# Kernel tuning notes

Measured on AMD Instinct MI355X. Metric: run time of the kernel, lower is better.

Reference implementation:

```python
import jax, jax.numpy as jnp
import numpy as np

IN_F = 256
OUT_F = 256
ALPHA = 0.2  # leakyrelu negative slope


def setup_inputs() -> dict:
    key = jax.random.key(0)
    k1, k2, k3 = jax.random.split(key, 3)
    B, N = 64, 1024
    x_loc = jax.random.normal(k1, (B, N, IN_F), dtype=jnp.float32)
    # xavier_uniform with gain=1.414
    def xavier(k, shape, gain=1.414):
        fan_in, fan_out = shape[0], shape[1]
        bound = gain * np.sqrt(6.0 / (fan_in + fan_out))
        return jax.random.uniform(k, shape, jnp.float32, -bound, bound)
    W = xavier(k2, (IN_F, OUT_F))
    a = xavier(k3, (2 * OUT_F, 1))
    return {"x_loc": x_loc, "W": W, "a": a, "entity_num": N}


def reference(x_loc, W, a, entity_num):
    # h: [B, N, F]
    h = jnp.matmul(x_loc, W)
    F_out = W.shape[1]
    a1 = a[:F_out, 0]   # [F]
    a2 = a[F_out:, 0]   # [F]
    # score(i, j) = leakyrelu(a1 . h_i + a2 . h_j)  -- decomposition of
    # matmul(cat(h_i, h_j), a); identical math, avoids O(N^2 * 2F) tensor.
    s1 = jnp.einsum('bnf,f->bn', h, a1)  # [B, N]
    s2 = jnp.einsum('bnf,f->bn', h, a2)  # [B, N]
    e = s1[:, :, None] + s2[:, None, :]  # [B, N, N]
    e = jnp.where(e > 0, e, ALPHA * e)   # leakyrelu(alpha=0.2)
    attention = jax.nn.softmax(e, axis=2)
    h_prime = jnp.matmul(attention, h)   # [B, N, F]
    return h_prime  # concat=False -> no elu
```

## Files before the change

kernel.cpp:

```cpp
#include <hip/hip_runtime.h>


typedef unsigned short u16;
typedef unsigned int   u32;
typedef float  f32x4  __attribute__((ext_vector_type(4)));
typedef __bf16 bf16x8 __attribute__((ext_vector_type(8)));
typedef __bf16 bf16x4 __attribute__((ext_vector_type(4)));

#define NB    64
#define NENT  1024
#define FD    256
#define NROWS (NB * NENT)
#define ALPHA 0.2f
#define LOG2E 1.4426950408889634f

typedef __attribute__((address_space(1))) const void* gas_ptr;
typedef __attribute__((address_space(3))) void*       las_ptr;
__device__ __forceinline__ void gload16(const void* g, void* l) {
  __builtin_amdgcn_global_load_lds((gas_ptr)g, (las_ptr)l, 16, 0, 0);
}
__device__ __forceinline__ float fexp2(float x) {
  float r;
  asm("v_exp_f32 %0, %1" : "=v"(r) : "v"(x));
  return r;
}

__global__ __launch_bounds__(256) void k_wa(const float* __restrict__ W,
                                            const float* __restrict__ a,
                                            float* __restrict__ Wa1,
                                            float* __restrict__ Wa2) {
  const int k = blockIdx.x, f = threadIdx.x;
  const float w = W[(size_t)k * FD + f];
  float p1 = w * a[f];
  float p2 = w * a[FD + f];
#pragma unroll
  for (int off = 1; off < 64; off <<= 1) {
    p1 += __shfl_xor(p1, off, 64);
    p2 += __shfl_xor(p2, off, 64);
  }
  __shared__ float r1[4], r2[4];
  const int wv = f >> 6, lane = f & 63;
  if (lane == 0) { r1[wv] = p1; r2[wv] = p2; }
  __syncthreads();
  if (f == 0) {
    Wa1[k] = r1[0] + r1[1] + r1[2] + r1[3];
    Wa2[k] = r2[0] + r2[1] + r2[2] + r2[3];
  }
}

__global__ __launch_bounds__(256) void k_wt(const float* __restrict__ W,
                                            u16* __restrict__ Wt) {
  __shared__ float tile[64][65];
  const int t = threadIdx.x;
  const int ki = blockIdx.x >> 2, fi = blockIdx.x & 3;
  const int k0 = ki * 64, f0 = fi * 64;
  const int r = t >> 4, c4 = (t & 15) * 4;
#pragma unroll
  for (int it = 0; it < 4; ++it) {
    const int row = r + it * 16;
    float4 v = *(const float4*)&W[(size_t)(k0 + row) * FD + f0 + c4];
    tile[row][c4 + 0] = v.x; tile[row][c4 + 1] = v.y;
    tile[row][c4 + 2] = v.z; tile[row][c4 + 3] = v.w;
  }
  __syncthreads();
#pragma unroll
  for (int it = 0; it < 4; ++it) {
    const int fr = r + it * 16;
    bf16x4 pk;
    pk[0] = (__bf16)tile[c4 + 0][fr]; pk[1] = (__bf16)tile[c4 + 1][fr];
    pk[2] = (__bf16)tile[c4 + 2][fr]; pk[3] = (__bf16)tile[c4 + 3][fr];
    *(bf16x4*)&Wt[(size_t)(f0 + fr) * FD + k0 + c4] = pk;
  }
}

__global__ __launch_bounds__(512, 2) void k_h(
    const float* __restrict__ x, const u16* __restrict__ Wt,
    const float* __restrict__ Wa1g, const float* __restrict__ Wa2g,
    u16* __restrict__ h_oct, float* __restrict__ s1, float* __restrict__ s2) {
  __shared__ __align__(16) u16 A_lds[2][4][256][8];
  __shared__ __align__(16) u16 B_lds[2][4][256][8];
  __shared__ float wa1[FD], wa2[FD];
  const int t = threadIdx.x;
  const int lane = t & 63, wv = t >> 6;
  const int wr = wv >> 2, wc = wv & 3;
  const int g16 = lane >> 4, c15 = lane & 15;
  const int p = blockIdx.x;
  const int lb = (p & 7) * 32 + (p >> 3);
  const int rT = lb * 256;
  if (t < FD) { wa1[t] = Wa1g[t]; wa2[t] = Wa2g[t]; }
  const int row = t >> 1, half = t & 1;
  const float* xsrc = x + (size_t)(rT + row) * FD + half * 16;
  float p1 = 0.f, p2 = 0.f;
  f32x4 acc[8][4];
  const f32x4 vz = {0.f, 0.f, 0.f, 0.f};
#pragma unroll
  for (int i = 0; i < 8; ++i)
#pragma unroll
    for (int j = 0; j < 4; ++j) acc[i][j] = vz;

  auto stage = [&](int nb, int kc, const float4& f0, const float4& f1,
                   const float4& f2, const float4& f3) {
    const int k0n = kc * 32;
    const int d0 = t;
    gload16(Wt + (size_t)(d0 & 255) * FD + k0n + (d0 >> 8) * 8,
            (char*)(&B_lds[nb][0][0][0]) + d0 * 16);
    const int d1 = t + 512;
    gload16(Wt + (size_t)(d1 & 255) * FD + k0n + (d1 >> 8) * 8,
            (char*)(&B_lds[nb][0][0][0]) + d1 * 16);
    bf16x8 w0, w1;
    w0[0] = (__bf16)f0.x; w0[1] = (__bf16)f0.y;
    w0[2] = (__bf16)f0.z; w0[3] = (__bf16)f0.w;
    w0[4] = (__bf16)f1.x; w0[5] = (__bf16)f1.y;
    w0[6] = (__bf16)f1.z; w0[7] = (__bf16)f1.w;
    w1[0] = (__bf16)f2.x; w1[1] = (__bf16)f2.y;
    w1[2] = (__bf16)f2.z; w1[3] = (__bf16)f2.w;
    w1[4] = (__bf16)f3.x; w1[5] = (__bf16)f3.y;
    w1[6] = (__bf16)f3.z; w1[7] = (__bf16)f3.w;
    *(bf16x8*)&A_lds[nb][half * 2][row][0] = w0;
    *(bf16x8*)&A_lds[nb][half * 2 + 1][row][0] = w1;
    const int kb = k0n + half * 16;
    p1 += f0.x*wa1[kb+ 0] + f0.y*wa1[kb+ 1] + f0.z*wa1[kb+ 2] + f0.w*wa1[kb+ 3]
        + f1.x*wa1[kb+ 4] + f1.y*wa1[kb+ 5] + f1.z*wa1[kb+ 6] + f1.w*wa1[kb+ 7]
        + f2.x*wa1[kb+ 8] + f2.y*wa1[kb+ 9] + f2.z*wa1[kb+10] + f2.w*wa1[kb+11]
        + f3.x*wa1[kb+12] + f3.y*wa1[kb+13] + f3.z*wa1[kb+14] + f3.w*wa1[kb+15];
    p2 += f0.x*wa2[kb+ 0] + f0.y*wa2[kb+ 1] + f0.z*wa2[kb+ 2] + f0.w*wa2[kb+ 3]
        + f1.x*wa2[kb+ 4] + f1.y*wa2[kb+ 5] + f1.z*wa2[kb+ 6] + f1.w*wa2[kb+ 7]
        + f2.x*wa2[kb+ 8] + f2.y*wa2[kb+ 9] + f2.z*wa2[kb+10] + f2.w*wa2[kb+11]
        + f3.x*wa2[kb+12] + f3.y*wa2[kb+13] + f3.z*wa2[kb+14] + f3.w*wa2[kb+15];
  };
  auto mfma_step = [&](int cb) {
    bf16x8 bfv[4];
#pragma unroll
    for (int fj = 0; fj < 4; ++fj)
      bfv[fj] = *(const bf16x8*)&B_lds[cb][g16][wc * 64 + fj * 16 + c15][0];
#pragma unroll
    for (int fi = 0; fi < 8; ++fi) {
      bf16x8 af = *(const bf16x8*)&A_lds[cb][g16][wr * 128 + fi * 16 + c15][0];
#pragma unroll
      for (int fj = 0; fj < 4; ++fj)
        acc[fi][fj] = __builtin_amdgcn_mfma_f32_16x16x32_bf16(
            af, bfv[fj], acc[fi][fj], 0, 0, 0);
    }
  };

  float4 xc0 = *(const float4*)(xsrc +  0);
  float4 xc1 = *(const float4*)(xsrc +  4);
  float4 xc2 = *(const float4*)(xsrc +  8);
  float4 xc3 = *(const float4*)(xsrc + 12);
  float4 xb0 = *(const float4*)(xsrc + 32);
  float4 xb1 = *(const float4*)(xsrc + 36);
  float4 xb2 = *(const float4*)(xsrc + 40);
  float4 xb3 = *(const float4*)(xsrc + 44);
  float4 xa0 = *(const float4*)(xsrc + 64);
  float4 xa1 = *(const float4*)(xsrc + 68);
  float4 xa2 = *(const float4*)(xsrc + 72);
  float4 xa3 = *(const float4*)(xsrc + 76);
  __syncthreads();
  stage(0, 0, xc0, xc1, xc2, xc3);
  __syncthreads();
#pragma unroll 1
  for (int ks2 = 0; ks2 < 4; ++ks2) {
    stage(1, 2 * ks2 + 1, xb0, xb1, xb2, xb3);
    if (2 * ks2 + 3 < 8) {
      const float* s = xsrc + (2 * ks2 + 3) * 32;
      xb0 = *(const float4*)(s);      xb1 = *(const float4*)(s + 4);
      xb2 = *(const float4*)(s + 8);  xb3 = *(const float4*)(s + 12);
    }
    mfma_step(0);
    __syncthreads();
    if (2 * ks2 + 2 < 8) {
      stage(0, 2 * ks2 + 2, xa0, xa1, xa2, xa3);
      if (2 * ks2 + 4 < 8) {
        const float* s = xsrc + (2 * ks2 + 4) * 32;
        xa0 = *(const float4*)(s);      xa1 = *(const float4*)(s + 4);
        xa2 = *(const float4*)(s + 8);  xa3 = *(const float4*)(s + 12);
      }
    }
    mfma_step(1);
    __syncthreads();
  }
  p1 += __shfl_xor(p1, 1, 64);
  p2 += __shfl_xor(p2, 1, 64);
  if (half == 0) { s1[rT + row] = p1; s2[rT + row] = p2; }
#pragma unroll
  for (int fi = 0; fi < 8; ++fi) {
    const int rowb = rT + wr * 128 + fi * 16 + 4 * g16;
    const int oct = rowb >> 3, u = rowb & 7;
#pragma unroll
    for (int fj = 0; fj < 4; ++fj) {
      const int col = wc * 64 + fj * 16 + c15;
      bf16x4 pk;
      pk[0] = (__bf16)acc[fi][fj][0]; pk[1] = (__bf16)acc[fi][fj][1];
      pk[2] = (__bf16)acc[fi][fj][2]; pk[3] = (__bf16)acc[fi][fj][3];
      *(bf16x4*)((u16*)h_oct + ((size_t)oct * FD + col) * 8 + u) = pk;
    }
  }
}

__global__ __launch_bounds__(512, 2) void k_pv(
    const u16* __restrict__ h_oct, const float* __restrict__ s1,
    const float* __restrict__ s2, float* __restrict__ out) {
  __shared__ __align__(16) u16 P_lds[2][4][256][8];
  __shared__ __align__(16) u16 V_lds[2][4][256][8];
  __shared__ float s2l[NENT];
  const int t = threadIdx.x;
  const int lane = t & 63, wv = t >> 6;
  const int wr = wv >> 2, wc = wv & 3;
  const int g16 = lane >> 4, c15 = lane & 15;
  const int p = blockIdx.x;
  const int lb = (p & 7) * 32 + (p >> 3);
  const int b = lb >> 2, itile = lb & 3;
  const int i0 = itile * 256;
  const int irow = t & 255, gsl = t >> 8;
  const int rowg = b * NENT + i0 + irow;
  const float s1v = s1[rowg];
  const size_t obase = (size_t)b * (NENT / 8);
  f32x4 acc[8][4];
  const f32x4 vz = {0.f, 0.f, 0.f, 0.f};
#pragma unroll
  for (int i = 0; i < 8; ++i)
#pragma unroll
    for (int j = 0; j < 4; ++j) acc[i][j] = vz;
  float zsum = 0.f;

  auto vload = [&](int nb, int ksn) {
    const int j0n = ksn * 32;
    const int d0 = t;
    gload16(h_oct + ((obase + (j0n >> 3) + (d0 >> 8)) * FD + (d0 & 255)) * 8,
            (char*)(&V_lds[nb][0][0][0]) + d0 * 16);
    const int d1 = t + 512;
    gload16(h_oct + ((obase + (j0n >> 3) + (d1 >> 8)) * FD + (d1 & 255)) * 8,
            (char*)(&V_lds[nb][0][0][0]) + d1 * 16);
  };

  vload(0, 0);
  *(float2*)&s2l[t * 2] = *(const float2*)&s2[(size_t)b * NENT + t * 2];
  __syncthreads();
  float sm = s2l[lane];
#pragma unroll
  for (int j = 1; j < 16; ++j) sm = fmaxf(sm, s2l[lane + j * 64]);
#pragma unroll
  for (int off = 1; off < 64; off <<= 1) sm = fmaxf(sm, __shfl_xor(sm, off, 64));
  const float q = s1v + sm;
  const float mv = fmaxf(q, ALPHA * q);
  const float C2v = ALPHA * LOG2E;
  const float mvC = mv * LOG2E;
  const float s1A = s1v * LOG2E - mvC;
  const float s1B = s1v * C2v - mvC;

  auto genp = [&](int nb, int ksn) {
    const int jb = ksn * 32 + gsl * 16;
    float4 qa = *(const float4*)&s2l[jb];
    float4 qb = *(const float4*)&s2l[jb + 4];
    float4 qc = *(const float4*)&s2l[jb + 8];
    float4 qd = *(const float4*)&s2l[jb + 12];
    float zp = 0.f;
    auto pg = [&](float s2j) -> float {
      float vA = fmaf(s2j, LOG2E, s1A);
      float vB = fmaf(s2j, C2v, s1B);
      float r = fexp2(fmaxf(vA, vB));
      zp += r;
      return r;
    };
    bf16x8 pw0, pw1;
    pw0[0] = (__bf16)pg(qa.x); pw0[1] = (__bf16)pg(qa.y);
    pw0[2] = (__bf16)pg(qa.z); pw0[3] = (__bf16)pg(qa.w);
    pw0[4] = (__bf16)pg(qb.x); pw0[5] = (__bf16)pg(qb.y);
    pw0[6] = (__bf16)pg(qb.z); pw0[7] = (__bf16)pg(qb.w);
    pw1[0] = (__bf16)pg(qc.x); pw1[1] = (__bf16)pg(qc.y);
    pw1[2] = (__bf16)pg(qc.z); pw1[3] = (__bf16)pg(qc.w);
    pw1[4] = (__bf16)pg(qd.x); pw1[5] = (__bf16)pg(qd.y);
    pw1[6] = (__bf16)pg(qd.z); pw1[7] = (__bf16)pg(qd.w);
    zsum += zp;
    *(bf16x8*)&P_lds[nb][2 * gsl][irow][0] = pw0;
    *(bf16x8*)&P_lds[nb][2 * gsl + 1][irow][0] = pw1;
  };
  auto mfma_step = [&](int cb) {
    bf16x8 bfv[4];
#pragma unroll
    for (int fj = 0; fj < 4; ++fj)
      bfv[fj] = *(const bf16x8*)&V_lds[cb][g16][wc * 64 + fj * 16 + c15][0];
#pragma unroll
    for (int fi = 0; fi < 8; ++fi) {
      bf16x8 af = *(const bf16x8*)&P_lds[cb][g16][wr * 128 + fi * 16 + c15][0];
#pragma unroll
      for (int fj = 0; fj < 4; ++fj)
        acc[fi][fj] = __builtin_amdgcn_mfma_f32_16x16x32_bf16(
            af, bfv[fj], acc[fi][fj], 0, 0, 0);
    }
  };

  genp(0, 0);
  __syncthreads();
#pragma unroll 1
  for (int ks2 = 0; ks2 < 16; ++ks2) {
    vload(1, 2 * ks2 + 1);
    genp(1, 2 * ks2 + 1);
    mfma_step(0);
    __syncthreads();
    if (2 * ks2 + 2 < 32) {
      vload(0, 2 * ks2 + 2);
      genp(0, 2 * ks2 + 2);
    }
    mfma_step(1);
    __syncthreads();
  }
  float* zred = (float*)&P_lds[0][0][0][0];
  zred[gsl * 256 + irow] = zsum;
  __syncthreads();
#pragma unroll
  for (int fi = 0; fi < 8; ++fi) {
    const int rloc = wr * 128 + fi * 16 + 4 * g16;
    float rz[4];
#pragma unroll
    for (int r = 0; r < 4; ++r)
      rz[r] = __builtin_amdgcn_rcpf(zred[rloc + r] + zred[256 + rloc + r]);
#pragma unroll
    for (int fj = 0; fj < 4; ++fj) {
      const int col = wc * 64 + fj * 16 + c15;
      float* o = out + ((size_t)b * NENT + i0 + rloc) * FD + col;
      o[0 * FD] = acc[fi][fj][0] * rz[0];
      o[1 * FD] = acc[fi][fj][1] * rz[1];
      o[2 * FD] = acc[fi][fj][2] * rz[2];
      o[3 * FD] = acc[fi][fj][3] * rz[3];
    }
  }
}

extern "C" void kernel_launch(void* const* d_in, const int* in_sizes, int n_in,
                              void* d_out, int out_size, void* d_ws, size_t ws_size,
                              hipStream_t stream) {
  const float* x = (const float*)d_in[0];
  const float* W = (const float*)d_in[1];
  const float* a = (const float*)d_in[2];
  float* out = (float*)d_out;

  char* ws = (char*)d_ws;
  u16*   h_oct = (u16*)ws;
  float* s1  = (float*)(ws + (size_t)33554432);
  float* s2  = s1 + NROWS;
  float* Wa1 = s2 + NROWS;
  float* Wa2 = Wa1 + FD;
  u16*   Wt  = (u16*)(Wa2 + FD);

  k_wa<<<dim3(256), dim3(256), 0, stream>>>(W, a, Wa1, Wa2);
  k_wt<<<dim3(16), dim3(256), 0, stream>>>(W, Wt);
  k_h<<<dim3(256), dim3(512), 0, stream>>>(x, Wt, Wa1, Wa2, h_oct, s1, s2);
  k_pv<<<dim3(256), dim3(512), 0, stream>>>(h_oct, s1, s2, out);
}
```

Before: 78.62 us.

## Deepen software pipelining with explicit waitcnt barriers and triple-buffered V tiles

Result: slower. 83.09 us (+5.7%).

```diff
diff --git a/kernel.cpp b/kernel.cpp
--- a/kernel.cpp
+++ b/kernel.cpp
@@ -13,6 +13,15 @@
 #define NROWS (NB * NENT)
 #define ALPHA 0.2f
 #define LOG2E 1.4426950408889634f
+
+#define VMCNT(n)  asm volatile("s_waitcnt vmcnt(" #n ")" ::: "memory")
+#define LGKMCNT0  asm volatile("s_waitcnt lgkmcnt(0)" ::: "memory")
+#define BAR()                                                                  \
+  do {                                                                         \
+    __builtin_amdgcn_s_barrier();                                              \
+    asm volatile("" ::: "memory");                                             \
+    __builtin_amdgcn_sched_barrier(0);                                         \
+  } while (0)
 
 typedef __attribute__((address_space(1))) const void* gas_ptr;
 typedef __attribute__((address_space(3))) void*       las_ptr;
@@ -87,7 +96,6 @@
   const int p = blockIdx.x;
   const int lb = (p & 7) * 32 + (p >> 3);
   const int rT = lb * 256;
-  if (t < FD) { wa1[t] = Wa1g[t]; wa2[t] = Wa2g[t]; }
   const int row = t >> 1, half = t & 1;
   const float* xsrc = x + (size_t)(rT + row) * FD + half * 16;
   float p1 = 0.f, p2 = 0.f;
@@ -98,8 +106,7 @@
 #pragma unroll
     for (int j = 0; j < 4; ++j) acc[i][j] = vz;
 
-  auto stage = [&](int nb, int kc, const float4& f0, const float4& f1,
-                   const float4& f2, const float4& f3) {
+  auto issueB = [&](int nb, int kc) {
     const int k0n = kc * 32;
     const int d0 = t;
     gload16(Wt + (size_t)(d0 & 255) * FD + k0n + (d0 >> 8) * 8,
@@ -107,32 +114,39 @@
     const int d1 = t + 512;
     gload16(Wt + (size_t)(d1 & 255) * FD + k0n + (d1 >> 8) * 8,
             (char*)(&B_lds[nb][0][0][0]) + d1 * 16);
+  };
+  auto stageA = [&](int nb, int kc, const float4* xr) {
     bf16x8 w0, w1;
-    w0[0] = (__bf16)f0.x; w0[1] = (__bf16)f0.y;
-    w0[2] = (__bf16)f0.z; w0[3] = (__bf16)f0.w;
-    w0[4] = (__bf16)f1.x; w0[5] = (__bf16)f1.y;
-    w0[6] = (__bf16)f1.z; w0[7] = (__bf16)f1.w;
-    w1[0] = (__bf16)f2.x; w1[1] = (__bf16)f2.y;
-    w1[2] = (__bf16)f2.z; w1[3] = (__bf16)f2.w;
-    w1[4] = (__bf16)f3.x; w1[5] = (__bf16)f3.y;
-    w1[6] = (__bf16)f3.z; w1[7] = (__bf16)f3.w;
+    w0[0] = (__bf16)xr[0].x; w0[1] = (__bf16)xr[0].y;
+    w0[2] = (__bf16)xr[0].z; w0[3] = (__bf16)xr[0].w;
+    w0[4] = (__bf16)xr[1].x; w0[5] = (__bf16)xr[1].y;
+    w0[6] = (__bf16)xr[1].z; w0[7] = (__bf16)xr[1].w;
+    w1[0] = (__bf16)xr[2].x; w1[1] = (__bf16)xr[2].y;
+    w1[2] = (__bf16)xr[2].z; w1[3] = (__bf16)xr[2].w;
+    w1[4] = (__bf16)xr[3].x; w1[5] = (__bf16)xr[3].y;
+    w1[6] = (__bf16)xr[3].z; w1[7] = (__bf16)xr[3].w;
     *(bf16x8*)&A_lds[nb][half * 2][row][0] = w0;
     *(bf16x8*)&A_lds[nb][half * 2 + 1][row][0] = w1;
-    const int kb = k0n + half * 16;
-    p1 += f0.x*wa1[kb+ 0] + f0.y*wa1[kb+ 1] + f0.z*wa1[kb+ 2] + f0.w*wa1[kb+ 3]
-        + f1.x*wa1[kb+ 4] + f1.y*wa1[kb+ 5] + f1.z*wa1[kb+ 6] + f1.w*wa1[kb+ 7]
-        + f2.x*wa1[kb+ 8] + f2.y*wa1[kb+ 9] + f2.z*wa1[kb+10] + f2.w*wa1[kb+11]
-        + f3.x*wa1[kb+12] + f3.y*wa1[kb+13] + f3.z*wa1[kb+14] + f3.w*wa1[kb+15];
-    p2 += f0.x*wa2[kb+ 0] + f0.y*wa2[kb+ 1] + f0.z*wa2[kb+ 2] + f0.w*wa2[kb+ 3]
-        + f1.x*wa2[kb+ 4] + f1.y*wa2[kb+ 5] + f1.z*wa2[kb+ 6] + f1.w*wa2[kb+ 7]
-        + f2.x*wa2[kb+ 8] + f2.y*wa2[kb+ 9] + f2.z*wa2[kb+10] + f2.w*wa2[kb+11]
-        + f3.x*wa2[kb+12] + f3.y*wa2[kb+13] + f3.z*wa2[kb+14] + f3.w*wa2[kb+15];
+    const int kb = kc * 32 + half * 16;
+#pragma unroll
+    for (int q = 0; q < 4; ++q) {
+      p1 += xr[q].x * wa1[kb + 4 * q + 0] + xr[q].y * wa1[kb + 4 * q + 1] +
+            xr[q].z * wa1[kb + 4 * q + 2] + xr[q].w * wa1[kb + 4 * q + 3];
+      p2 += xr[q].x * wa2[kb + 4 * q + 0] + xr[q].y * wa2[kb + 4 * q + 1] +
+            xr[q].z * wa2[kb + 4 * q + 2] + xr[q].w * wa2[kb + 4 * q + 3];
+    }
+  };
+  auto loadx = [&](float4* xr, int kc) {
+    const float* s = xsrc + kc * 32;
+    xr[0] = *(const float4*)(s);      xr[1] = *(const float4*)(s + 4);
+    xr[2] = *(const float4*)(s + 8);  xr[3] = *(const float4*)(s + 12);
   };
   auto mfma_step = [&](int cb) {
     bf16x8 bfv[4];
 #pragma unroll
     for (int fj = 0; fj < 4; ++fj)
       bfv[fj] = *(const bf16x8*)&B_lds[cb][g16][wc * 64 + fj * 16 + c15][0];
+    __builtin_amdgcn_s_setprio(1);
 #pragma unroll
     for (int fi = 0; fi < 8; ++fi) {
       bf16x8 af = *(const bf16x8*)&A_lds[cb][g16][wr * 128 + fi * 16 + c15][0];
@@ -141,43 +155,36 @@
         acc[fi][fj] = __builtin_amdgcn_mfma_f32_16x16x32_bf16(
             af, bfv[fj], acc[fi][fj], 0, 0, 0);
     }
-  };
-
-  float4 xc0 = *(const float4*)(xsrc +  0);
-  float4 xc1 = *(const float4*)(xsrc +  4);
-  float4 xc2 = *(const float4*)(xsrc +  8);
-  float4 xc3 = *(const float4*)(xsrc + 12);
-  float4 xb0 = *(const float4*)(xsrc + 32);
-  float4 xb1 = *(const float4*)(xsrc + 36);
-  float4 xb2 = *(const float4*)(xsrc + 40);
-  float4 xb3 = *(const float4*)(xsrc + 44);
-  float4 xa0 = *(const float4*)(xsrc + 64);
-  float4 xa1 = *(const float4*)(xsrc + 68);
-  float4 xa2 = *(const float4*)(xsrc + 72);
-  float4 xa3 = *(const float4*)(xsrc + 76);
-  __syncthreads();
-  stage(0, 0, xc0, xc1, xc2, xc3);
-  __syncthreads();
-#pragma unroll 1
-  for (int ks2 = 0; ks2 < 4; ++ks2) {
-    stage(1, 2 * ks2 + 1, xb0, xb1, xb2, xb3);
-    if (2 * ks2 + 3 < 8) {
-      const float* s = xsrc + (2 * ks2 + 3) * 32;
-      xb0 = *(const float4*)(s);      xb1 = *(const float4*)(s + 4);
-      xb2 = *(const float4*)(s + 8);  xb3 = *(const float4*)(s + 12);
-    }
-    mfma_step(0);
-    __syncthreads();
-    if (2 * ks2 + 2 < 8) {
-      stage(0, 2 * ks2 + 2, xa0, xa1, xa2, xa3);
-      if (2 * ks2 + 4 < 8) {
-        const float* s = xsrc + (2 * ks2 + 4) * 32;
-        xa0 = *(const float4*)(s);      xa1 = *(const float4*)(s + 4);
-        xa2 = *(const float4*)(s + 8);  xa3 = *(const float4*)(s + 12);
-      }
-    }
-    mfma_step(1);
-    __syncthreads();
+    __builtin_amdgcn_s_setprio(0);
+  };
+
+  if (t < FD) { wa1[t] = Wa1g[t]; wa2[t] = Wa2g[t]; }
+  float4 xe[4], xo[4];
+  loadx(xe, 0);
+  loadx(xo, 1);
+  issueB(0, 0);
+  LGKMCNT0;
+  BAR();
+  stageA(0, 0, xe);
+  loadx(xe, 2);
+  LGKMCNT0;
+  VMCNT(4);
+  BAR();
+
+#pragma unroll
+  for (int k = 0; k < 8; ++k) {
+    if (k < 7) {
+      issueB((k + 1) & 1, k + 1);
+      float4* xr = (k & 1) ? xe : xo;
+      stageA((k + 1) & 1, k + 1, xr);
+      if (k + 3 < 8) loadx(xr, k + 3);
+    }
+    mfma_step(k & 1);
+    if (k < 7) {
+      LGKMCNT0;
+      if (k + 3 < 8) VMCNT(4); else VMCNT(0);
+      BAR();
+    }
   }
   p1 += __shfl_xor(p1, 1, 64);
   p2 += __shfl_xor(p2, 1, 64);
@@ -201,7 +208,7 @@
     const u16* __restrict__ h_oct, const float* __restrict__ s1,
     const float* __restrict__ s2, float* __restrict__ out) {
   __shared__ __align__(16) u16 P_lds[2][4][256][8];
-  __shared__ __align__(16) u16 V_lds[2][4][256][8];
+  __shared__ __align__(16) u16 V_lds[3][4][256][8];
   __shared__ float s2l[NENT];
   const int t = threadIdx.x;
   const int lane = t & 63, wv = t >> 6;
@@ -213,7 +220,6 @@
   const int i0 = itile * 256;
   const int irow = t & 255, gsl = t >> 8;
   const int rowg = b * NENT + i0 + irow;
-  const float s1v = s1[rowg];
   const size_t obase = (size_t)b * (NENT / 8);
   f32x4 acc[8][4];
   const f32x4 vz = {0.f, 0.f, 0.f, 0.f};
@@ -233,9 +239,13 @@
             (char*)(&V_lds[nb][0][0][0]) + d1 * 16);
   };
 
+  const float s1v = s1[rowg];
+  float2 s2f = *(const float2*)&s2[(size_t)b * NENT + t * 2];
   vload(0, 0);
-  *(float2*)&s2l[t * 2] = *(const float2*)&s2[(size_t)b * NENT + t * 2];
-  __syncthreads();
+  vload(1, 1);
+  *(float2*)&s2l[t * 2] = s2f;
+  LGKMCNT0;
+  BAR();
   float sm = s2l[lane];
 #pragma unroll
   for (int j = 1; j < 16; ++j) sm = fmaxf(sm, s2l[lane + j * 64]);
@@ -275,36 +285,44 @@
     *(bf16x8*)&P_lds[nb][2 * gsl][irow][0] = pw0;
     *(bf16x8*)&P_lds[nb][2 * gsl + 1][irow][0] = pw1;
   };
-  auto mfma_step = [&](int cb) {
+  auto mfma_step = [&](int pb, int vb) {
     bf16x8 bfv[4];
 #pragma unroll
     for (int fj = 0; fj < 4; ++fj)
-      bfv[fj] = *(const bf16x8*)&V_lds[cb][g16][wc * 64 + fj * 16 + c15][0];
+      bfv[fj] = *(const bf16x8*)&V_lds[vb][g16][wc * 64 + fj * 16 + c15][0];
+    __builtin_amdgcn_s_setprio(1);
 #pragma unroll
     for (int fi = 0; fi < 8; ++fi) {
-      bf16x8 af = *(const bf16x8*)&P_lds[cb][g16][wr * 128 + fi * 16 + c15][0];
+      bf16x8 af = *(const bf16x8*)&P_lds[pb][g16][wr * 128 + fi * 16 + c15][0];
 #pragma unroll
       for (int fj = 0; fj < 4; ++fj)
         acc[fi][fj] = __builtin_amdgcn_mfma_f32_16x16x32_bf16(
             af, bfv[fj], acc[fi][fj], 0, 0, 0);
     }
+    __builtin_amdgcn_s_setprio(0);
   };
 
   genp(0, 0);
+  LGKMCNT0;
+  VMCNT(2);
+  BAR();
+
+  int rb = 0, wb = 2;
+#pragma unroll 1
+  for (int k = 0; k < 32; ++k) {
+    if (k < 30) vload(wb, k + 2);
+    if (k < 31) genp((k + 1) & 1, k + 1);
+    mfma_step(k & 1, rb);
+    if (k < 31) {
+      LGKMCNT0;
+      if (k < 30) VMCNT(2);
+      else        VMCNT(0);
+      BAR();
+    }
+    rb = (rb == 2) ? 0 : rb + 1;
+    wb = (wb == 2) ? 0 : wb + 1;
+  }
   __syncthreads();
-#pragma unroll 1
-  for (int ks2 = 0; ks2 < 16; ++ks2) {
-    vload(1, 2 * ks2 + 1);
-    genp(1, 2 * ks2 + 1);
-    mfma_step(0);
-    __syncthreads();
-    if (2 * ks2 + 2 < 32) {
-      vload(0, 2 * ks2 + 2);
-      genp(0, 2 * ks2 + 2);
-    }
-    mfma_step(1);
-    __syncthreads();
-  }
   float* zred = (float*)&P_lds[0][0][0][0];
   zred[gsl * 256 + irow] = zsum;
   __syncthreads();
```

## Replace quadratic attention with sorted prefix-sum scan over rank-one scores

Applied to the files above, without the earlier changes.

Result: slower. 192.1 us (+144.3%).

```diff
diff --git a/kernel.cpp b/kernel.cpp
--- a/kernel.cpp
+++ b/kernel.cpp
@@ -12,17 +12,11 @@
 #define FD    256
 #define NROWS (NB * NENT)
 #define ALPHA 0.2f
-#define LOG2E 1.4426950408889634f
 
 typedef __attribute__((address_space(1))) const void* gas_ptr;
 typedef __attribute__((address_space(3))) void*       las_ptr;
 __device__ __forceinline__ void gload16(const void* g, void* l) {
   __builtin_amdgcn_global_load_lds((gas_ptr)g, (las_ptr)l, 16, 0, 0);
-}
-__device__ __forceinline__ float fexp2(float x) {
-  float r;
-  asm("v_exp_f32 %0, %1" : "=v"(r) : "v"(x));
-  return r;
 }
 
 __global__ __launch_bounds__(256) void k_wa(const float* __restrict__ W,
@@ -76,10 +70,12 @@
 __global__ __launch_bounds__(512, 2) void k_h(
     const float* __restrict__ x, const u16* __restrict__ Wt,
     const float* __restrict__ Wa1g, const float* __restrict__ Wa2g,
-    u16* __restrict__ h_oct, float* __restrict__ s1, float* __restrict__ s2) {
-  __shared__ __align__(16) u16 A_lds[2][4][256][8];
-  __shared__ __align__(16) u16 B_lds[2][4][256][8];
-  __shared__ float wa1[FD], wa2[FD];
+    u16* __restrict__ h, float* __restrict__ s1, float* __restrict__ s2) {
+  __shared__ __align__(16) char smem[67584];
+  u16* Ab = (u16*)smem;
+  u16* Bb = (u16*)(smem + 32768);
+  float* wa1 = (float*)(smem + 65536);
+  float* wa2 = wa1 + FD;
   const int t = threadIdx.x;
   const int lane = t & 63, wv = t >> 6;
   const int wr = wv >> 2, wc = wv & 3;
@@ -103,10 +99,10 @@
     const int k0n = kc * 32;
     const int d0 = t;
     gload16(Wt + (size_t)(d0 & 255) * FD + k0n + (d0 >> 8) * 8,
-            (char*)(&B_lds[nb][0][0][0]) + d0 * 16);
+            (char*)Bb + nb * 8192 * 2 + d0 * 16);
     const int d1 = t + 512;
     gload16(Wt + (size_t)(d1 & 255) * FD + k0n + (d1 >> 8) * 8,
-            (char*)(&B_lds[nb][0][0][0]) + d1 * 16);
+            (char*)Bb + nb * 8192 * 2 + d1 * 16);
     bf16x8 w0, w1;
     w0[0] = (__bf16)f0.x; w0[1] = (__bf16)f0.y;
     w0[2] = (__bf16)f0.z; w0[3] = (__bf16)f0.w;
@@ -116,8 +112,8 @@
     w1[2] = (__bf16)f2.z; w1[3] = (__bf16)f2.w;
     w1[4] = (__bf16)f3.x; w1[5] = (__bf16)f3.y;
     w1[6] = (__bf16)f3.z; w1[7] = (__bf16)f3.w;
-    *(bf16x8*)&A_lds[nb][half * 2][row][0] = w0;
-    *(bf16x8*)&A_lds[nb][half * 2 + 1][row][0] = w1;
+    *(bf16x8*)(Ab + ((nb * 4 + half * 2) * 256 + row) * 8) = w0;
+    *(bf16x8*)(Ab + ((nb * 4 + half * 2 + 1) * 256 + row) * 8) = w1;
     const int kb = k0n + half * 16;
     p1 += f0.x*wa1[kb+ 0] + f0.y*wa1[kb+ 1] + f0.z*wa1[kb+ 2] + f0.w*wa1[kb+ 3]
         + f1.x*wa1[kb+ 4] + f1.y*wa1[kb+ 5] + f1.z*wa1[kb+ 6] + f1.w*wa1[kb+ 7]
@@ -132,10 +128,10 @@
     bf16x8 bfv[4];
 #pragma unroll
     for (int fj = 0; fj < 4; ++fj)
-      bfv[fj] = *(const bf16x8*)&B_lds[cb][g16][wc * 64 + fj * 16 + c15][0];
+      bfv[fj] = *(const bf16x8*)(Bb + ((cb * 4 + g16) * 256 + wc * 64 + fj * 16 + c15) * 8);
 #pragma unroll
     for (int fi = 0; fi < 8; ++fi) {
-      bf16x8 af = *(const bf16x8*)&A_lds[cb][g16][wr * 128 + fi * 16 + c15][0];
+      bf16x8 af = *(const bf16x8*)(Ab + ((cb * 4 + g16) * 256 + wr * 128 + fi * 16 + c15) * 8);
 #pragma unroll
       for (int fj = 0; fj < 4; ++fj)
         acc[fi][fj] = __builtin_amdgcn_mfma_f32_16x16x32_bf16(
@@ -182,147 +178,224 @@
   p1 += __shfl_xor(p1, 1, 64);
   p2 += __shfl_xor(p2, 1, 64);
   if (half == 0) { s1[rT + row] = p1; s2[rT + row] = p2; }
-#pragma unroll
-  for (int fi = 0; fi < 8; ++fi) {
-    const int rowb = rT + wr * 128 + fi * 16 + 4 * g16;
-    const int oct = rowb >> 3, u = rowb & 7;
-#pragma unroll
-    for (int fj = 0; fj < 4; ++fj) {
-      const int col = wc * 64 + fj * 16 + c15;
-      bf16x4 pk;
-      pk[0] = (__bf16)acc[fi][fj][0]; pk[1] = (__bf16)acc[fi][fj][1];
-      pk[2] = (__bf16)acc[fi][fj][2]; pk[3] = (__bf16)acc[fi][fj][3];
-      *(bf16x4*)((u16*)h_oct + ((size_t)oct * FD + col) * 8 + u) = pk;
-    }
-  }
-}
-
-__global__ __launch_bounds__(512, 2) void k_pv(
-    const u16* __restrict__ h_oct, const float* __restrict__ s1,
+  u16* ep = (u16*)smem;
+#pragma unroll 1
+  for (int hh = 0; hh < 4; ++hh) {
+    if (wr == (hh >> 1)) {
+#pragma unroll
+      for (int fi2 = 0; fi2 < 4; ++fi2) {
+        const int fi = (hh & 1) * 4 + fi2;
+        const int erow = fi2 * 16 + 4 * g16;
+#pragma unroll
+        for (int fj = 0; fj < 4; ++fj) {
+          const int col = wc * 64 + fj * 16 + c15;
+#pragma unroll
+          for (int r = 0; r < 4; ++r) {
+            __bf16 bv = (__bf16)acc[fi][fj][r];
+            ep[(erow + r) * 264 + col] = __builtin_bit_cast(u16, bv);
+          }
+        }
+      }
+    }
+    __syncthreads();
+    const int rrow = t >> 3, seg = t & 7;
+    const u16* src = ep + rrow * 264 + seg * 32;
+    u16* dst = h + (size_t)(rT + hh * 64 + rrow) * FD + seg * 32;
+#pragma unroll
+    for (int q = 0; q < 4; ++q)
+      *(uint4*)(dst + q * 8) = *(const uint4*)(src + q * 8);
+    __syncthreads();
+  }
+}
+
+__global__ __launch_bounds__(512) void k_sc(
+    const u16* __restrict__ h, const float* __restrict__ s1,
     const float* __restrict__ s2, float* __restrict__ out) {
-  __shared__ __align__(16) u16 P_lds[2][4][256][8];
-  __shared__ __align__(16) u16 V_lds[2][4][256][8];
-  __shared__ float s2l[NENT];
+  __shared__ float key[1024];
+  __shared__ u16   pid[1024];
+  __shared__ float e2l[1024], e2al[1024];
+  __shared__ float Su[1025], Sv[1025];
+  __shared__ float c1l[1024], c2l[1024];
+  __shared__ u32   cnt[1025];
+  __shared__ u16   ibl[1025];
+  __shared__ u16   iol[1024];
+  __shared__ float UpS[8];
+  __shared__ float Up[8][64], Vp[8][64];
   const int t = threadIdx.x;
-  const int lane = t & 63, wv = t >> 6;
-  const int wr = wv >> 2, wc = wv & 3;
-  const int g16 = lane >> 4, c15 = lane & 15;
-  const int p = blockIdx.x;
-  const int lb = (p & 7) * 32 + (p >> 3);
-  const int b = lb >> 2, itile = lb & 3;
-  const int i0 = itile * 256;
-  const int irow = t & 255, gsl = t >> 8;
-  const int rowg = b * NENT + i0 + irow;
-  const float s1v = s1[rowg];
-  const size_t obase = (size_t)b * (NENT / 8);
-  f32x4 acc[8][4];
-  const f32x4 vz = {0.f, 0.f, 0.f, 0.f};
-#pragma unroll
-  for (int i = 0; i < 8; ++i)
-#pragma unroll
-    for (int j = 0; j < 4; ++j) acc[i][j] = vz;
-  float zsum = 0.f;
-
-  auto vload = [&](int nb, int ksn) {
-    const int j0n = ksn * 32;
-    const int d0 = t;
-    gload16(h_oct + ((obase + (j0n >> 3) + (d0 >> 8)) * FD + (d0 & 255)) * 8,
-            (char*)(&V_lds[nb][0][0][0]) + d0 * 16);
-    const int d1 = t + 512;
-    gload16(h_oct + ((obase + (j0n >> 3) + (d1 >> 8)) * FD + (d1 & 255)) * 8,
-            (char*)(&V_lds[nb][0][0][0]) + d1 * 16);
+  const int b = blockIdx.y, fc = blockIdx.x;
+  const int w = t >> 6, lane = t & 63;
+
+  key[t]       = s2[(size_t)b * NENT + t];       pid[t]       = (u16)t;
+  key[t + 512] = s2[(size_t)b * NENT + t + 512]; pid[t + 512] = (u16)(t + 512);
+  __syncthreads();
+  for (int kk = 2; kk <= 1024; kk <<= 1) {
+    for (int j = kk >> 1; j > 0; j >>= 1) {
+      if (j >= 64) __syncthreads();
+      else asm volatile("" ::: "memory");
+      const int i  = ((t & ~(j - 1)) << 1) | (t & (j - 1));
+      const int ix = i | j;
+      const bool up = ((i & kk) == 0);
+      float a = key[i], c = key[ix];
+      u16 pa = pid[i], pc = pid[ix];
+      const bool sw = up ? (a > c) : (a < c);
+      if (sw) { key[i] = c; key[ix] = a; pid[i] = pc; pid[ix] = pa; }
+    }
+  }
+  __syncthreads();
+  {
+    float k0 = key[t], k1 = key[t + 512];
+    e2l[t] = __expf(k0);        e2l[t + 512] = __expf(k1);
+    e2al[t] = __expf(ALPHA * k0); e2al[t + 512] = __expf(ALPHA * k1);
+  }
+  __syncthreads();
+  auto scanx = [&](const float* src, float* dst) {
+    float a = src[2 * t], bb = src[2 * t + 1];
+    float s = a + bb;
+    float inc = s;
+#pragma unroll
+    for (int d = 1; d < 64; d <<= 1) {
+      float o = __shfl_up(inc, d, 64);
+      if (lane >= d) inc += o;
+    }
+    if (lane == 63) UpS[w] = inc;
+    __syncthreads();
+    float woff = 0.f;
+#pragma unroll
+    for (int w2 = 0; w2 < 8; ++w2) { float pv = UpS[w2]; if (w2 < w) woff += pv; }
+    float P = woff + inc - s;
+    dst[2 * t] = P; dst[2 * t + 1] = P + a;
+    if (t == 511) dst[1024] = P + s;
+    __syncthreads();
   };
-
-  vload(0, 0);
-  *(float2*)&s2l[t * 2] = *(const float2*)&s2[(size_t)b * NENT + t * 2];
-  __syncthreads();
-  float sm = s2l[lane];
-#pragma unroll
-  for (int j = 1; j < 16; ++j) sm = fmaxf(sm, s2l[lane + j * 64]);
-#pragma unroll
-  for (int off = 1; off < 64; off <<= 1) sm = fmaxf(sm, __shfl_xor(sm, off, 64));
-  const float q = s1v + sm;
-  const float mv = fmaxf(q, ALPHA * q);
-  const float C2v = ALPHA * LOG2E;
-  const float mvC = mv * LOG2E;
-  const float s1A = s1v * LOG2E - mvC;
-  const float s1B = s1v * C2v - mvC;
-
-  auto genp = [&](int nb, int ksn) {
-    const int jb = ksn * 32 + gsl * 16;
-    float4 qa = *(const float4*)&s2l[jb];
-    float4 qb = *(const float4*)&s2l[jb + 4];
-    float4 qc = *(const float4*)&s2l[jb + 8];
-    float4 qd = *(const float4*)&s2l[jb + 12];
-    float zp = 0.f;
-    auto pg = [&](float s2j) -> float {
-      float vA = fmaf(s2j, LOG2E, s1A);
-      float vB = fmaf(s2j, C2v, s1B);
-      float r = fexp2(fmaxf(vA, vB));
-      zp += r;
-      return r;
-    };
-    bf16x8 pw0, pw1;
-    pw0[0] = (__bf16)pg(qa.x); pw0[1] = (__bf16)pg(qa.y);
-    pw0[2] = (__bf16)pg(qa.z); pw0[3] = (__bf16)pg(qa.w);
-    pw0[4] = (__bf16)pg(qb.x); pw0[5] = (__bf16)pg(qb.y);
-    pw0[6] = (__bf16)pg(qb.z); pw0[7] = (__bf16)pg(qb.w);
-    pw1[0] = (__bf16)pg(qc.x); pw1[1] = (__bf16)pg(qc.y);
-    pw1[2] = (__bf16)pg(qc.z); pw1[3] = (__bf16)pg(qc.w);
-    pw1[4] = (__bf16)pg(qd.x); pw1[5] = (__bf16)pg(qd.y);
-    pw1[6] = (__bf16)pg(qd.z); pw1[7] = (__bf16)pg(qd.w);
-    zsum += zp;
-    *(bf16x8*)&P_lds[nb][2 * gsl][irow][0] = pw0;
-    *(bf16x8*)&P_lds[nb][2 * gsl + 1][irow][0] = pw1;
+  scanx(e2l, Su);
+  scanx(e2al, Sv);
+  const float s2max = key[1023];
+  const float SuN = Su[1024], SvN = Sv[1024];
+  int kfA, kfB;
+  {
+    cnt[t] = 0; cnt[t + 512] = 0;
+    if (t == 0) cnt[1024] = 0;
+  }
+  __syncthreads();
+#pragma unroll
+  for (int hi = 0; hi < 2; ++hi) {
+    const int i = t + hi * 512;
+    const float s1v = s1[(size_t)b * NENT + i];
+    const float th = -s1v;
+    int kf = 0;
+#pragma unroll
+    for (int d = 1024; d >= 1; d >>= 1)
+      if (kf + d <= 1024 && key[kf + d - 1] < th) kf += d;
+    const float qm = s1v + s2max;
+    const float m = fmaxf(qm, ALPHA * qm);
+    const float en1 = __expf(fminf(s1v - m, 80.f));
+    const float en2 = __expf(fminf(ALPHA * s1v - m, 80.f));
+    const float Z = en1 * (SuN - Su[kf]) + en2 * Sv[kf];
+    const float rZ = 1.f / Z;
+    c1l[i] = en1 * rZ; c2l[i] = en2 * rZ;
+    if (hi == 0) kfA = kf; else kfB = kf;
+    atomicAdd(&cnt[kf], 1u);
+  }
+  __syncthreads();
+  {
+    float a = (float)cnt[2 * t], bb = (float)cnt[2 * t + 1];
+    cnt[2 * t] = 0; cnt[2 * t + 1] = 0;
+    if (t == 0) cnt[1024] = 0;
+    float s = a + bb;
+    float inc = s;
+#pragma unroll
+    for (int d = 1; d < 64; d <<= 1) {
+      float o = __shfl_up(inc, d, 64);
+      if (lane >= d) inc += o;
+    }
+    if (lane == 63) UpS[w] = inc;
+    __syncthreads();
+    float woff = 0.f;
+#pragma unroll
+    for (int w2 = 0; w2 < 8; ++w2) { float pv = UpS[w2]; if (w2 < w) woff += pv; }
+    float P = woff + inc - s;
+    ibl[2 * t] = (u16)P; ibl[2 * t + 1] = (u16)(P + a);
+    if (t == 511) ibl[1024] = (u16)(P + s);
+  }
+  __syncthreads();
+  {
+    int pos = (int)ibl[kfA] + (int)atomicAdd(&cnt[kfA], 1u);
+    pos = pos < 1023 ? pos : 1023;
+    iol[pos] = (u16)t;
+    int posB = (int)ibl[kfB] + (int)atomicAdd(&cnt[kfB], 1u);
+    posB = posB < 1023 ? posB : 1023;
+    iol[posB] = (u16)(t + 512);
+  }
+  __syncthreads();
+  const int col = fc * 64 + lane;
+  const u16* hb = h + (size_t)b * NENT * FD + col;
+  const int r0 = w * 128;
+  float ha[8], hc[8];
+  auto ldg8 = [&](float* dstv, int rbase) {
+#pragma unroll
+    for (int u = 0; u < 8; ++u) {
+      u16 raw = hb[(size_t)((int)pid[rbase + u]) * FD];
+      dstv[u] = (float)__builtin_bit_cast(__bf16, raw);
+    }
   };
-  auto mfma_step = [&](int cb) {
-    bf16x8 bfv[4];
-#pragma unroll
-    for (int fj = 0; fj < 4; ++fj)
-      bfv[fj] = *(const bf16x8*)&V_lds[cb][g16][wc * 64 + fj * 16 + c15][0];
-#pragma unroll
-    for (int fi = 0; fi < 8; ++fi) {
-      bf16x8 af = *(const bf16x8*)&P_lds[cb][g16][wr * 128 + fi * 16 + c15][0];
-#pragma unroll
-      for (int fj = 0; fj < 4; ++fj)
-        acc[fi][fj] = __builtin_amdgcn_mfma_f32_16x16x32_bf16(
-            af, bfv[fj], acc[fi][fj], 0, 0, 0);
-    }
-  };
-
-  genp(0, 0);
-  __syncthreads();
+  float U = 0.f, V = 0.f;
+  ldg8(ha, r0);
 #pragma unroll 1
-  for (int ks2 = 0; ks2 < 16; ++ks2) {
-    vload(1, 2 * ks2 + 1);
-    genp(1, 2 * ks2 + 1);
-    mfma_step(0);
-    __syncthreads();
-    if (2 * ks2 + 2 < 32) {
-      vload(0, 2 * ks2 + 2);
-      genp(0, 2 * ks2 + 2);
-    }
-    mfma_step(1);
-    __syncthreads();
-  }
-  float* zred = (float*)&P_lds[0][0][0][0];
-  zred[gsl * 256 + irow] = zsum;
-  __syncthreads();
-#pragma unroll
-  for (int fi = 0; fi < 8; ++fi) {
-    const int rloc = wr * 128 + fi * 16 + 4 * g16;
-    float rz[4];
-#pragma unroll
-    for (int r = 0; r < 4; ++r)
-      rz[r] = __builtin_amdgcn_rcpf(zred[rloc + r] + zred[256 + rloc + r]);
-#pragma unroll
-    for (int fj = 0; fj < 4; ++fj) {
-      const int col = wc * 64 + fj * 16 + c15;
-      float* o = out + ((size_t)b * NENT + i0 + rloc) * FD + col;
-      o[0 * FD] = acc[fi][fj][0] * rz[0];
-      o[1 * FD] = acc[fi][fj][1] * rz[1];
-      o[2 * FD] = acc[fi][fj][2] * rz[2];
-      o[3 * FD] = acc[fi][fj][3] * rz[3];
+  for (int g = 0; g < 8; ++g) {
+    const int rb = r0 + g * 16;
+    ldg8(hc, rb + 8);
+#pragma unroll
+    for (int u = 0; u < 8; ++u) {
+      U += e2l[rb + u] * ha[u]; V += e2al[rb + u] * ha[u];
+    }
+    if (g < 7) ldg8(ha, rb + 16);
+#pragma unroll
+    for (int u = 0; u < 8; ++u) {
+      U += e2l[rb + 8 + u] * hc[u]; V += e2al[rb + 8 + u] * hc[u];
+    }
+  }
+  Up[w][lane] = U; Vp[w][lane] = V;
+  __syncthreads();
+  float Uoff = 0.f, Voff = 0.f, UN = 0.f, VN = 0.f;
+#pragma unroll
+  for (int w2 = 0; w2 < 8; ++w2) {
+    float a = Up[w2][lane], c = Vp[w2][lane];
+    if (w2 < w) { Uoff += a; Voff += c; }
+    UN += a; VN += c;
+  }
+  U = Uoff; V = Voff;
+  ldg8(ha, r0);
+#pragma unroll 1
+  for (int g = 0; g < 8; ++g) {
+    const int rb = r0 + g * 16;
+    ldg8(hc, rb + 8);
+#pragma unroll
+    for (int u = 0; u < 8; ++u) {
+      const int r = rb + u;
+      const int e0 = ibl[r], e1 = ibl[r + 1];
+      for (int idx = e0; idx < e1; ++idx) {
+        const int i = iol[idx];
+        out[((size_t)b * NENT + i) * FD + col] = c1l[i] * (UN - U) + c2l[i] * V;
+      }
+      U += e2l[r] * ha[u]; V += e2al[r] * ha[u];
+    }
+    if (g < 7) ldg8(ha, rb + 16);
+#pragma unroll
+    for (int u = 0; u < 8; ++u) {
+      const int r = rb + 8 + u;
+      const int e0 = ibl[r], e1 = ibl[r + 1];
+      for (int idx = e0; idx < e1; ++idx) {
+        const int i = iol[idx];
+        out[((size_t)b * NENT + i) * FD + col] = c1l[i] * (UN - U) + c2l[i] * V;
+      }
+      U += e2l[r] * hc[u]; V += e2al[r] * hc[u];
+    }
+  }
+  if (w == 7) {
+    const int e0 = ibl[1024];
+    for (int idx = e0; idx < 1024; ++idx) {
+      const int i = iol[idx];
+      out[((size_t)b * NENT + i) * FD + col] = c1l[i] * (UN - U) + c2l[i] * V;
     }
   }
 }
@@ -336,7 +409,7 @@
   float* out = (float*)d_out;
 
   char* ws = (char*)d_ws;
-  u16*   h_oct = (u16*)ws;
+  u16*   h   = (u16*)ws;
   float* s1  = (float*)(ws + (size_t)33554432);
   float* s2  = s1 + NROWS;
   float* Wa1 = s2 + NROWS;
@@ -345,6 +418,6 @@
 
   k_wa<<<dim3(256), dim3(256), 0, stream>>>(W, a, Wa1, Wa2);
   k_wt<<<dim3(16), dim3(256), 0, stream>>>(W, Wt);
-  k_h<<<dim3(256), dim3(512), 0, stream>>>(x, Wt, Wa1, Wa2, h_oct, s1, s2);
-  k_pv<<<dim3(256), dim3(512), 0, stream>>>(h_oct, s1, s2, out);
-}
+  k_h<<<dim3(256), dim3(512), 0, stream>>>(x, Wt, Wa1, Wa2, h, s1, s2);
+  k_sc<<<dim3(4, NB), dim3(512), 0, stream>>>(h, s1, s2, out);
+}
```
